# Kernel optimization log

Hardware: AMD Instinct MI355X
Metric: run time of the kernel (lower is better)

The kernel has to match this reference:

```python
import jax, jax.numpy as jnp
import numpy as np
import math

INPUT_DIM = 1024
EMBED_DIM = 1024
NUM_HEADS = 16
HEAD_DIM = EMBED_DIM // NUM_HEADS


def setup_inputs() -> dict:
    key = jax.random.key(0)
    k_x, k_qkv, k_out_w, k_out_b = jax.random.split(key, 4)
    x = jax.random.normal(k_x, (1, 4096, INPUT_DIM), dtype=jnp.float32)
    # nn.Linear weights are [out, in]; kaiming-uniform-ish scale
    s1 = 1.0 / math.sqrt(INPUT_DIM)
    s2 = 1.0 / math.sqrt(EMBED_DIM)
    qkv_w = jax.random.uniform(k_qkv, (3 * EMBED_DIM, INPUT_DIM), jnp.float32, -s1, s1)
    out_w = jax.random.uniform(k_out_w, (EMBED_DIM, EMBED_DIM), jnp.float32, -s2, s2)
    out_b = jax.random.uniform(k_out_b, (EMBED_DIM,), jnp.float32, -s2, s2)
    return {"x": x, "qkv_w": qkv_w, "out_w": out_w, "out_b": out_b}


def reference(x, qkv_w, out_w, out_b):
    B, N, C = x.shape
    qkv = jnp.einsum('bnc,ec->bne', x, qkv_w)  # [B,N,3E]
    q = qkv[:, :, 0:EMBED_DIM].reshape(B, N, NUM_HEADS, HEAD_DIM)
    k = qkv[:, :, EMBED_DIM:2 * EMBED_DIM].reshape(B, N, NUM_HEADS, HEAD_DIM)
    v = qkv[:, :, 2 * EMBED_DIM:].reshape(B, N, NUM_HEADS, HEAD_DIM)
    scores = jnp.einsum('bihd,bjhd->bhij', q, k) / jnp.sqrt(jnp.float32(HEAD_DIM))
    attn = jax.nn.softmax(scores, axis=-1)  # [B,H,N,N]
    out = jnp.einsum('bhik,bkhd->bhid', attn, v)
    out = out.transpose(0, 2, 1, 3).reshape(B, N, EMBED_DIM)
    return jnp.einsum('bne,fe->bnf', out, out_w) + out_b
```

## Files before the change

kernel.cpp:

```cpp
#include <hip/hip_runtime.h>
#include <hip/hip_bf16.h>

typedef __bf16 bf16;
typedef bf16 bf16x8 __attribute__((ext_vector_type(8)));
typedef bf16 bf16x4 __attribute__((ext_vector_type(4)));
typedef float f32x4 __attribute__((ext_vector_type(4)));

#define MFMA16(a, b, c) __builtin_amdgcn_mfma_f32_16x16x32_bf16(a, b, c, 0, 0, 0)

__device__ __forceinline__ void g2l16(const bf16* g, bf16* l) {
  __builtin_amdgcn_global_load_lds(
      (__attribute__((address_space(1))) void*)(void*)g,
      (__attribute__((address_space(3))) void*)l,
      16, 0, 0);
}

__global__ void sniff_dtype(const void* __restrict__ x, int* __restrict__ flag) {
  const unsigned short* u = (const unsigned short*)x;
  const int lane = threadIdx.x;
  unsigned short v = u[lane];
  int e = (v >> 7) & 0xFF;
  int sane = (e == 0) || (e >= 112 && e <= 142);
  unsigned long long m = __ballot(sane);
  if (lane == 0) flag[0] = (__popcll(m) >= 56) ? 1 : 0;
}

__global__ void convert_to_bf16(const void* __restrict__ in, bf16* __restrict__ out,
                                long n8, const int* __restrict__ flag) {
  long i = (long)blockIdx.x * 256 + threadIdx.x;
  if (i >= n8) return;
  if (*flag) {
    ((bf16x8*)out)[i] = ((const bf16x8*)in)[i];
  } else {
    const float4* p = (const float4*)in;
    float4 a = p[i * 2], b = p[i * 2 + 1];
    bf16x8 v;
    v[0] = (bf16)a.x; v[1] = (bf16)a.y; v[2] = (bf16)a.z; v[3] = (bf16)a.w;
    v[4] = (bf16)b.x; v[5] = (bf16)b.y; v[6] = (bf16)b.z; v[7] = (bf16)b.w;
    ((bf16x8*)out)[i] = v;
  }
}

__global__ __launch_bounds__(256) void gemm_qkv(
    const bf16* __restrict__ A, const bf16* __restrict__ B,
    bf16* __restrict__ qB, bf16* __restrict__ kP, bf16* __restrict__ vP) {
  __shared__ __align__(16) bf16 As[128 * 32];
  __shared__ __align__(16) bf16 Bs[128 * 32];

  const int tid  = threadIdx.x;
  const int lane = tid & 63;
  const int wave = tid >> 6;
  const int wm   = wave >> 1, wn = wave & 1;
  const int l15  = lane & 15, quad = lane >> 4;
  const long m0 = (long)blockIdx.x * 128;
  const long n0 = (long)blockIdx.y * 128;
  const int  K  = 1024;

  const bf16* Ab = A + m0 * K;
  const bf16* Bb = B + n0 * K;
  const int rowA = tid & 127;
  const int dc   = tid >> 7;

  f32x4 acc[4][4] = {};

  for (int k0 = 0; k0 < K; k0 += 32) {
    g2l16(Ab + (long)rowA * K + k0 + dc * 8,       As + tid * 8);
    g2l16(Ab + (long)rowA * K + k0 + (dc + 2) * 8, As + (tid + 256) * 8);
    g2l16(Bb + (long)rowA * K + k0 + dc * 8,       Bs + tid * 8);
    g2l16(Bb + (long)rowA * K + k0 + (dc + 2) * 8, Bs + (tid + 256) * 8);
    __syncthreads();

    bf16x8 af[4], bfr[4];
#pragma unroll
    for (int t = 0; t < 4; t++) {
      af[t]  = *(const bf16x8*)(As + (quad * 128 + wm * 64 + t * 16 + l15) * 8);
      bfr[t] = *(const bf16x8*)(Bs + (quad * 128 + wn * 64 + t * 16 + l15) * 8);
    }
#pragma unroll
    for (int tm = 0; tm < 4; tm++)
#pragma unroll
      for (int tn = 0; tn < 4; tn++)
        acc[tm][tn] = MFMA16(af[tm], bfr[tn], acc[tm][tn]);
    __syncthreads();
  }

  const long rb = m0 + wm * 64;
  const long cb = n0 + wn * 64;
  const int third = (int)(n0 >> 10);
  const float QSC = 0.125f * 1.44269504088896f;

#pragma unroll
  for (int tm = 0; tm < 4; tm++) {
#pragma unroll
    for (int tn = 0; tn < 4; tn++) {
      const long r0 = rb + tm * 16 + quad * 4;
      const long c  = cb + tn * 16 + l15;
      if (third == 0) {
#pragma unroll
        for (int r = 0; r < 4; r++)
          qB[(r0 + r) * 1024 + c] = (bf16)(acc[tm][tn][r] * QSC);
      } else if (third == 1) {
        const int ep = (int)c - 1024;
        const int h = ep >> 6, d = ep & 63;
        const long bhd = (long)h * 64 * 4096 + (long)((d >> 3) * 64) * 8 + (d & 7);
#pragma unroll
        for (int r = 0; r < 4; r++) {
          const int n = (int)(r0 + r);
          const int kt = n >> 6, kpos = n & 63;
          const int tn_ = 2 * (kpos >> 5) + ((kpos >> 2) & 1);
          const int m   = tn_ * 16 + ((kpos >> 3) & 3) * 4 + (kpos & 3);
          kP[bhd + (long)kt * 4096 + m * 8] = (bf16)acc[tm][tn][r];
        }
      } else {
        const int ep = (int)c - 2048;
        const int h = ep >> 6, d = ep & 63;
#pragma unroll
        for (int r = 0; r < 4; r++) {
          const int n = (int)(r0 + r);
          const int kt = n >> 6, pc = (n & 63) >> 3, j = n & 7;
          vP[(long)(h * 64 + kt) * 4096 + (pc * 64 + d) * 8 + j] = (bf16)acc[tm][tn][r];
        }
      }
    }
  }
}

template <bool BIAS, bool DYNOUT>
__global__ __launch_bounds__(256) void gemm_bt(
    const bf16* __restrict__ A, const bf16* __restrict__ B,
    void* __restrict__ Cv, const bf16* __restrict__ bias,
    int M, int Nn, int K, const int* __restrict__ oflag) {
  __shared__ __align__(16) bf16 As[128 * 32];
  __shared__ __align__(16) bf16 Bs[128 * 32];

  const int tid  = threadIdx.x;
  const int lane = tid & 63;
  const int wave = tid >> 6;
  const int wm   = wave >> 1, wn = wave & 1;
  const int l15  = lane & 15, quad = lane >> 4;
  const long m0 = (long)blockIdx.x * 128;
  const long n0 = (long)blockIdx.y * 128;

  const bf16* Ab = A + m0 * K;
  const bf16* Bb = B + n0 * K;
  const int rowA = tid & 127;
  const int dc   = tid >> 7;

  f32x4 acc[4][4] = {};

  for (int k0 = 0; k0 < K; k0 += 32) {
    g2l16(Ab + (long)rowA * K + k0 + dc * 8,       As + tid * 8);
    g2l16(Ab + (long)rowA * K + k0 + (dc + 2) * 8, As + (tid + 256) * 8);
    g2l16(Bb + (long)rowA * K + k0 + dc * 8,       Bs + tid * 8);
    g2l16(Bb + (long)rowA * K + k0 + (dc + 2) * 8, Bs + (tid + 256) * 8);
    __syncthreads();

    bf16x8 af[4], bfr[4];
#pragma unroll
    for (int t = 0; t < 4; t++) {
      af[t]  = *(const bf16x8*)(As + (quad * 128 + wm * 64 + t * 16 + l15) * 8);
      bfr[t] = *(const bf16x8*)(Bs + (quad * 128 + wn * 64 + t * 16 + l15) * 8);
    }
#pragma unroll
    for (int tm = 0; tm < 4; tm++)
#pragma unroll
      for (int tn = 0; tn < 4; tn++)
        acc[tm][tn] = MFMA16(af[tm], bfr[tn], acc[tm][tn]);
    __syncthreads();
  }

  const int obf = DYNOUT ? *oflag : 1;
  const long rb = m0 + wm * 64;
  const long cb = n0 + wn * 64;
#pragma unroll
  for (int tm = 0; tm < 4; tm++) {
#pragma unroll
    for (int tn = 0; tn < 4; tn++) {
      const long r0 = rb + tm * 16 + quad * 4;
      const long c  = cb + tn * 16 + l15;
      const float bv = BIAS ? (float)bias[c] : 0.0f;
#pragma unroll
      for (int r = 0; r < 4; r++) {
        const float val = acc[tm][tn][r] + bv;
        const long idx = (r0 + r) * Nn + c;
        if (DYNOUT && !obf) ((float*)Cv)[idx] = val;
        else                ((bf16*)Cv)[idx]  = (bf16)val;
      }
    }
  }
}

__global__ __launch_bounds__(256) void flash_attn(
    const bf16* __restrict__ qB, const bf16* __restrict__ kP,
    const bf16* __restrict__ vP, bf16* __restrict__ O) {
  __shared__ __align__(16) bf16 Ks[2][64 * 64];
  __shared__ __align__(16) bf16 Vs[2][64 * 64];

  const int tid = threadIdx.x;
  const int lane = tid & 63;
  const int wave = tid >> 6;
  const int l15 = lane & 15, quad = lane >> 4;
  const int qt = blockIdx.x, h = blockIdx.y;
  const int q0 = qt * 128;

  bf16x8 qf[2][2];
#pragma unroll
  for (int g = 0; g < 2; g++) {
    const bf16* qrow = qB + (long)(q0 + wave * 32 + g * 16 + l15) * 1024 + h * 64;
    qf[g][0] = *(const bf16x8*)(qrow + quad * 8);
    qf[g][1] = *(const bf16x8*)(qrow + 32 + quad * 8);
  }

  f32x4 oa[2][4] = {};
  float l_sum[2] = {0.0f, 0.0f};

  const bf16* kb = kP + (long)h * 64 * 4096;
  const bf16* vb = vP + (long)h * 64 * 4096;

#pragma unroll
  for (int i = 0; i < 2; i++) {
    g2l16(kb + (tid + i * 256) * 8, Ks[0] + (tid + i * 256) * 8);
    g2l16(vb + (tid + i * 256) * 8, Vs[0] + (tid + i * 256) * 8);
  }

  for (int kt = 0; kt < 64; kt++) {
    const int cur = kt & 1;
    __syncthreads();
    if (kt + 1 < 64) {
      const bf16* kbase = kb + (long)(kt + 1) * 4096;
      const bf16* vbase = vb + (long)(kt + 1) * 4096;
#pragma unroll
      for (int i = 0; i < 2; i++) {
        g2l16(kbase + (tid + i * 256) * 8, Ks[cur ^ 1] + (tid + i * 256) * 8);
        g2l16(vbase + (tid + i * 256) * 8, Vs[cur ^ 1] + (tid + i * 256) * 8);
      }
    }

    f32x4 s[2][4];
#pragma unroll
    for (int tn = 0; tn < 4; tn++) {
      bf16x8 a0 = *(const bf16x8*)(Ks[cur] + ((quad)*64 + tn * 16 + l15) * 8);
      bf16x8 a1 = *(const bf16x8*)(Ks[cur] + ((4 + quad) * 64 + tn * 16 + l15) * 8);
      f32x4 z0 = {}; z0 = MFMA16(a0, qf[0][0], z0); z0 = MFMA16(a1, qf[0][1], z0);
      f32x4 z1 = {}; z1 = MFMA16(a0, qf[1][0], z1); z1 = MFMA16(a1, qf[1][1], z1);
      s[0][tn] = z0; s[1][tn] = z1;
    }

    bf16x8 pf[2][2];
#pragma unroll
    for (int g = 0; g < 2; g++)
#pragma unroll
      for (int tn = 0; tn < 4; tn++)
#pragma unroll
        for (int r = 0; r < 4; r++) {
          float p = __builtin_amdgcn_exp2f(s[g][tn][r]);
          l_sum[g] += p;
          pf[g][tn >> 1][(tn & 1) * 4 + r] = (bf16)p;
        }

#pragma unroll
    for (int tm = 0; tm < 4; tm++) {
      bf16x8 v0 = *(const bf16x8*)(Vs[cur] + ((quad)*64 + tm * 16 + l15) * 8);
      bf16x8 v1 = *(const bf16x8*)(Vs[cur] + ((4 + quad) * 64 + tm * 16 + l15) * 8);
      oa[0][tm] = MFMA16(v0, pf[0][0], oa[0][tm]);
      oa[0][tm] = MFMA16(v1, pf[0][1], oa[0][tm]);
      oa[1][tm] = MFMA16(v0, pf[1][0], oa[1][tm]);
      oa[1][tm] = MFMA16(v1, pf[1][1], oa[1][tm]);
    }
  }

#pragma unroll
  for (int g = 0; g < 2; g++) {
    float l = l_sum[g];
    l += __shfl_xor(l, 16, 64);
    l += __shfl_xor(l, 32, 64);
    const float inv = 1.0f / l;
    bf16* orow = O + (long)(q0 + wave * 32 + g * 16 + l15) * 1024 + h * 64;
#pragma unroll
    for (int tm = 0; tm < 4; tm++) {
      bf16x4 v;
#pragma unroll
      for (int r = 0; r < 4; r++) v[r] = (bf16)(oa[g][tm][r] * inv);
      *(bf16x4*)(orow + tm * 16 + quad * 4) = v;
    }
  }
}

extern "C" void kernel_launch(void* const* d_in, const int* in_sizes, int n_in,
                              void* d_out, int out_size, void* d_ws, size_t ws_size,
                              hipStream_t stream) {
  const void* x     = d_in[0];
  const void* qkv_w = d_in[1];
  const void* out_w = d_in[2];
  const void* out_b = d_in[3];

  char* ws = (char*)d_ws;
  int*  flag = (int*)ws;
  bf16* qB   = (bf16*)(ws + 4096);
  bf16* kP   = (bf16*)(ws + 4096 + 8388608);
  bf16* vP   = (bf16*)(ws + 4096 + 16777216);
  bf16* ob   = (bf16*)(ws + 4096 + 25165824);
  bf16* qwb  = (bf16*)(ws + 4096 + 33554432);
  bf16* xb   = ob;
  bf16* owb  = qB;
  bf16* obb  = qB + 1048576;

  sniff_dtype<<<1, 64, 0, stream>>>(x, flag);
  convert_to_bf16<<<2048, 256, 0, stream>>>(x, xb, 524288, flag);
  convert_to_bf16<<<1536, 256, 0, stream>>>(qkv_w, qwb, 393216, flag);

  gemm_qkv<<<dim3(32, 24), 256, 0, stream>>>(xb, qwb, qB, kP, vP);

  flash_attn<<<dim3(32, 16), 256, 0, stream>>>(qB, kP, vP, ob);

  convert_to_bf16<<<512, 256, 0, stream>>>(out_w, owb, 131072, flag);
  convert_to_bf16<<<1, 256, 0, stream>>>(out_b, obb, 128, flag);

  gemm_bt<true, true><<<dim3(32, 8), 256, 0, stream>>>(
      ob, owb, d_out, obb, 4096, 1024, 1024, flag);
}
```

Baseline: 266.7 us.

## Compute softmax row sums via MFMA, remap attention blocks per XCD, vectorize V stores

The attention kernel now accumulates the softmax denominator with extra MFMAs against a ones vector. This replaces the per-element VALU adds and the final cross-lane shuffles. The grid is flattened so that blocks for the same head land on the same XCD, which is meant to improve L2 reuse of K/V. The QKV GEMM epilogue writes V in 4-element bf16 vector stores instead of scalar stores. In exchange it adds four MFMAs per key tile and relies on row alignment assumptions in the V layout.

```diff
diff --git a/kernel.cpp b/kernel.cpp
--- a/kernel.cpp
+++ b/kernel.cpp
@@ -114,12 +114,13 @@
       } else {
         const int ep = (int)c - 2048;
         const int h = ep >> 6, d = ep & 63;
-#pragma unroll
-        for (int r = 0; r < 4; r++) {
-          const int n = (int)(r0 + r);
-          const int kt = n >> 6, pc = (n & 63) >> 3, j = n & 7;
-          vP[(long)(h * 64 + kt) * 4096 + (pc * 64 + d) * 8 + j] = (bf16)acc[tm][tn][r];
-        }
+        const int n0r = (int)r0;
+        const int kt = n0r >> 6, pc = (n0r & 63) >> 3;
+        bf16x4 v;
+#pragma unroll
+        for (int r = 0; r < 4; r++) v[r] = (bf16)acc[tm][tn][r];
+        *(bf16x4*)(vP + (long)(h * 64 + kt) * 4096 + (pc * 64 + d) * 8 +
+                   (quad & 1) * 4) = v;
       }
     }
   }
@@ -200,7 +201,10 @@
   const int lane = tid & 63;
   const int wave = tid >> 6;
   const int l15 = lane & 15, quad = lane >> 4;
-  const int qt = blockIdx.x, h = blockIdx.y;
+  const int bid = blockIdx.x;
+  const int xcd = bid & 7, bi = bid >> 3;
+  const int h  = xcd + 8 * (bi >> 5);
+  const int qt = bi & 31;
   const int q0 = qt * 128;
 
   bf16x8 qf[2][2];
@@ -211,8 +215,12 @@
     qf[g][1] = *(const bf16x8*)(qrow + 32 + quad * 8);
   }
 
+  bf16x8 onesf;
+#pragma unroll
+  for (int j = 0; j < 8; j++) onesf[j] = (bf16)1.0f;
+
   f32x4 oa[2][4] = {};
-  float l_sum[2] = {0.0f, 0.0f};
+  f32x4 la[2] = {};
 
   const bf16* kb = kP + (long)h * 64 * 4096;
   const bf16* vb = vP + (long)h * 64 * 4096;
@@ -252,11 +260,9 @@
 #pragma unroll
       for (int tn = 0; tn < 4; tn++)
 #pragma unroll
-        for (int r = 0; r < 4; r++) {
-          float p = __builtin_amdgcn_exp2f(s[g][tn][r]);
-          l_sum[g] += p;
-          pf[g][tn >> 1][(tn & 1) * 4 + r] = (bf16)p;
-        }
+        for (int r = 0; r < 4; r++)
+          pf[g][tn >> 1][(tn & 1) * 4 + r] =
+              (bf16)__builtin_amdgcn_exp2f(s[g][tn][r]);
 
 #pragma unroll
     for (int tm = 0; tm < 4; tm++) {
@@ -267,14 +273,16 @@
       oa[1][tm] = MFMA16(v0, pf[1][0], oa[1][tm]);
       oa[1][tm] = MFMA16(v1, pf[1][1], oa[1][tm]);
     }
+#pragma unroll
+    for (int g = 0; g < 2; g++) {
+      la[g] = MFMA16(onesf, pf[g][0], la[g]);
+      la[g] = MFMA16(onesf, pf[g][1], la[g]);
+    }
   }
 
 #pragma unroll
   for (int g = 0; g < 2; g++) {
-    float l = l_sum[g];
-    l += __shfl_xor(l, 16, 64);
-    l += __shfl_xor(l, 32, 64);
-    const float inv = 1.0f / l;
+    const float inv = 1.0f / la[g][0];
     bf16* orow = O + (long)(q0 + wave * 32 + g * 16 + l15) * 1024 + h * 64;
 #pragma unroll
     for (int tm = 0; tm < 4; tm++) {
@@ -311,7 +319,7 @@
 
   gemm_qkv<<<dim3(32, 24), 256, 0, stream>>>(xb, qwb, qB, kP, vP);
 
-  flash_attn<<<dim3(32, 16), 256, 0, stream>>>(qB, kP, vP, ob);
+  flash_attn<<<512, 256, 0, stream>>>(qB, kP, vP, ob);
 
   convert_to_bf16<<<512, 256, 0, stream>>>(out_w, owb, 131072, flag);
   convert_to_bf16<<<1, 256, 0, stream>>>(out_b, obb, 128, flag);
```

New measurement: 269.7 us. Within noise of the previous version (+1.1%).
